# Kernel optimization log

Hardware: AMD Instinct MI355X
Metric: run time of the kernel (lower is better)

## Reference

```python
import jax, jax.numpy as jnp
import numpy as np

NEG_SLOPE = 0.2  # PyG GATConv leaky_relu slope


def _add_self_loops(edge_index, num_nodes):
    loops = jnp.arange(num_nodes, dtype=edge_index.dtype)
    src = jnp.concatenate([edge_index[0], loops])
    dst = jnp.concatenate([edge_index[1], loops])
    return src, dst


def _gat_conv(x, src, dst, W, a_src, a_dst, b, num_nodes):
    # W: [in, H*F]; a_src, a_dst: [H, F]; b: [H*F]
    H, F = a_src.shape
    h = (x @ W).reshape(num_nodes, H, F)                # [N,H,F]
    alpha_src = jnp.einsum('nhf,hf->nh', h, a_src)      # [N,H]
    alpha_dst = jnp.einsum('nhf,hf->nh', h, a_dst)      # [N,H]
    logits = alpha_src[src] + alpha_dst[dst]            # [E,H]
    logits = jax.nn.leaky_relu(logits, NEG_SLOPE)
    # segment softmax over incoming edges of each dst node
    seg_max = jax.ops.segment_max(logits, dst, num_segments=num_nodes)  # [N,H]
    e = jnp.exp(logits - seg_max[dst])                  # [E,H]
    denom = jax.ops.segment_sum(e, dst, num_segments=num_nodes)         # [N,H]
    alpha = e / denom[dst]                              # [E,H] (self-loops guarantee denom>0)
    msg = h[src] * alpha[:, :, None]                    # [E,H,F]
    out = jax.ops.segment_sum(msg, dst, num_segments=num_nodes)         # [N,H,F]
    return out.reshape(num_nodes, H * F) + b            # concat=True


def _gcn_conv(x, src, dst, W, b, num_nodes):
    h = x @ W                                           # [N,out]
    ones = jnp.ones(dst.shape[0], dtype=h.dtype)
    deg = jax.ops.segment_sum(ones, dst, num_segments=num_nodes)        # [N]
    dinv = jnp.where(deg > 0, jax.lax.rsqrt(deg), 0.0)
    norm = dinv[src] * dinv[dst]                        # [E]
    out = jax.ops.segment_sum(h[src] * norm[:, None], dst, num_segments=num_nodes)
    return out + b


def setup_inputs() -> dict:
    key = jax.random.key(0)
    ks = jax.random.split(key, 10)
    N, E = 50000, 800000
    in_dim, hid, H1, ncls = 128, 32, 8, 16
    s = 0.05
    d = {}
    d['x'] = jax.random.normal(ks[0], (N, in_dim), jnp.float32)
    d['edge_index'] = jax.random.randint(ks[1], (2, E), 0, N)
    # GATConv 1: in=128 -> hid=32, heads=8
    d['W1'] = jax.random.normal(ks[2], (in_dim, H1 * hid), jnp.float32) * s
    d['a_src1'] = jax.random.normal(ks[3], (H1, hid), jnp.float32) * s
    d['a_dst1'] = jax.random.normal(ks[4], (H1, hid), jnp.float32) * s
    d['b1'] = jnp.zeros((H1 * hid,), jnp.float32)
    # GATConv 2: in=256 -> hid//2=16, heads=1
    d['W2'] = jax.random.normal(ks[5], (H1 * hid, hid // 2), jnp.float32) * s
    d['a_src2'] = jax.random.normal(ks[6], (1, hid // 2), jnp.float32) * s
    d['a_dst2'] = jax.random.normal(ks[7], (1, hid // 2), jnp.float32) * s
    d['b2'] = jnp.zeros((hid // 2,), jnp.float32)
    # GCNConv: 16 -> 16 classes
    d['W3'] = jax.random.normal(ks[8], (hid // 2, ncls), jnp.float32) * s
    d['b3'] = jnp.zeros((ncls,), jnp.float32)
    return d


def reference(x, edge_index, W1, a_src1, a_dst1, b1, W2, a_src2, a_dst2, b2, W3, b3):
    N = x.shape[0]
    src, dst = _add_self_loops(edge_index, N)
    # dropout layers are identity in eval mode
    h = _gat_conv(x, src, dst, W1, a_src1, a_dst1, b1, N)
    h = jax.nn.elu(h)
    h = _gat_conv(h, src, dst, W2, a_src2, a_dst2, b2, N)
    h = jax.nn.elu(h)
    out = _gcn_conv(h, src, dst, W3, b3, N)
    return out
```

## Files before the change

kernel.cpp:

```cpp
#include <hip/hip_runtime.h>
#include <hip/hip_bf16.h>
#include <math.h>

#define NEG_SLOPE 0.2f
#define DEG_CAP 64

typedef float f32x4 __attribute__((ext_vector_type(4)));
typedef short bf16x8 __attribute__((ext_vector_type(8)));
typedef unsigned int u32x2 __attribute__((ext_vector_type(2)));

static __device__ __forceinline__ float lrelu(float x) { return x > 0.f ? x : NEG_SLOPE * x; }
static __device__ __forceinline__ float elu1(float x)  { return x > 0.f ? x : (expf(x) - 1.f); }

static __device__ __forceinline__ unsigned short f2bf(float x) {
    __hip_bfloat16 h = __float2bfloat16(x);
    return *reinterpret_cast<unsigned short*>(&h);
}
static __device__ __forceinline__ unsigned int pack2bf(float a, float b) {
    return (unsigned int)f2bf(a) | ((unsigned int)f2bf(b) << 16);
}
static __device__ __forceinline__ float bflo(unsigned int u) { return __uint_as_float(u << 16); }
static __device__ __forceinline__ float bfhi(unsigned int u) { return __uint_as_float(u & 0xFFFF0000u); }

__global__ void fill_kernel(const int* __restrict__ ei, int* __restrict__ fillc,
                            int* __restrict__ srcs_p, int E, int E2) {
    int i = blockIdx.x * blockDim.x + threadIdx.x;
    if (i >= E2) return;
    int src, dst;
    if (i < E) { src = ei[i]; dst = ei[E + i]; }
    else       { src = i - E; dst = i - E; }
    int pos = atomicAdd(&fillc[dst], 1);
    if (pos < DEG_CAP) srcs_p[(size_t)dst * DEG_CAP + pos] = src;
}

__global__ __launch_bounds__(256) void prep_kernel(const int* __restrict__ fillc, int* __restrict__ cnts,
                                                   float* __restrict__ dinv, const float* __restrict__ W1,
                                                   unsigned short* __restrict__ Wb, int N) {
    int i = blockIdx.x * 256 + threadIdx.x;
    if (i < N) {
        int c = fillc[i];
        cnts[i] = c < DEG_CAP ? c : DEG_CAP;
        dinv[i] = rsqrtf((float)c);
    }
    if (i < 32768) {
        int j = i & 7, lane = (i >> 3) & 63, t = (i >> 9) & 15, kk = i >> 13;
        int k = kk * 32 + (lane >> 4) * 8 + j;
        int n = t * 16 + (lane & 15);
        Wb[i] = f2bf(W1[k * 256 + n]);
    }
}

__global__ __launch_bounds__(256) void gemm1_kernel(const float* __restrict__ x, const unsigned short* __restrict__ Wb,
                                                    const float* __restrict__ a_src, const float* __restrict__ a_dst,
                                                    unsigned short* __restrict__ h1b, float* __restrict__ as1,
                                                    float* __restrict__ ad1, int M) {
    int w = threadIdx.x >> 6, lane = threadIdx.x & 63;
    int quad = lane >> 4, c = lane & 15;
    int rowA = blockIdx.x * 64 + w * 16 + c;
    int rowAc = rowA < M ? rowA : M - 1;
    f32x4 acc[16];
    #pragma unroll
    for (int t = 0; t < 16; t++) acc[t] = (f32x4){0.f, 0.f, 0.f, 0.f};
    #pragma unroll
    for (int kk = 0; kk < 4; kk++) {
        const float* ap = &x[(size_t)rowAc * 128 + kk * 32 + quad * 8];
        float4 a0 = *(const float4*)ap;
        float4 a1 = *(const float4*)(ap + 4);
        union { bf16x8 v; unsigned int u[4]; } af;
        af.u[0] = pack2bf(a0.x, a0.y); af.u[1] = pack2bf(a0.z, a0.w);
        af.u[2] = pack2bf(a1.x, a1.y); af.u[3] = pack2bf(a1.z, a1.w);
        const bf16x8* bp = (const bf16x8*)&Wb[(size_t)(kk * 16) * 512 + lane * 8];
        #pragma unroll
        for (int t = 0; t < 16; t++) {
            bf16x8 bf = bp[t * 64];
            acc[t] = __builtin_amdgcn_mfma_f32_16x16x32_bf16(af.v, bf, acc[t], 0, 0, 0);
        }
    }
    int growb = blockIdx.x * 64 + w * 16 + quad * 4;
    #pragma unroll
    for (int r = 0; r < 4; r++) {
        int grow = growb + r;
        if (grow < M) {
            #pragma unroll
            for (int t = 0; t < 16; t++)
                h1b[(size_t)grow * 256 + t * 16 + c] = f2bf(acc[t][r]);
        }
    }
    float asA[8], asB[8], adA[8], adB[8];
    #pragma unroll
    for (int h = 0; h < 8; h++) {
        asA[h] = a_src[h * 32 + c];      asB[h] = a_src[h * 32 + 16 + c];
        adA[h] = a_dst[h * 32 + c];      adB[h] = a_dst[h * 32 + 16 + c];
    }
    #pragma unroll
    for (int r = 0; r < 4; r++) {
        int grow = growb + r;
        #pragma unroll
        for (int h = 0; h < 8; h++) {
            float ps = acc[2 * h][r] * asA[h] + acc[2 * h + 1][r] * asB[h];
            float pd = acc[2 * h][r] * adA[h] + acc[2 * h + 1][r] * adB[h];
            ps += __shfl_xor(ps, 1); ps += __shfl_xor(ps, 2); ps += __shfl_xor(ps, 4); ps += __shfl_xor(ps, 8);
            pd += __shfl_xor(pd, 1); pd += __shfl_xor(pd, 2); pd += __shfl_xor(pd, 4); pd += __shfl_xor(pd, 8);
            if (c == 0 && grow < M) { as1[grow * 8 + h] = ps; ad1[grow * 8 + h] = pd; }
        }
    }
}

__global__ __launch_bounds__(256) void agg1_kernel(const unsigned short* __restrict__ h1b, const float* __restrict__ asrc,
                                                   const float* __restrict__ adst, const int* __restrict__ cnts,
                                                   const int* __restrict__ srcs_p, const float* __restrict__ b1,
                                                   unsigned short* __restrict__ h1pb, int N) {
    int node = blockIdx.x * 4 + (threadIdx.x >> 6);
    if (node >= N) return;
    int lane = threadIdx.x & 63;
    int h = lane >> 3, e8 = lane & 7;
    float adn = adst[node * 8 + h];
    int cnt = cnts[node];
    float4 acc = make_float4(0.f, 0.f, 0.f, 0.f);
    float den = 0.f;
    int o4 = lane * 4;
    int sv = srcs_p[node * DEG_CAP + (lane < cnt ? lane : cnt - 1)];
    int g = 0;
    for (; g + 16 <= cnt; g += 16) {
        int ssA = __shfl(sv, g + e8);
        int ssB = __shfl(sv, g + 8 + e8);
        float wA = __expf(lrelu(asrc[ssA * 8 + h] + adn));
        float wB = __expf(lrelu(asrc[ssB * 8 + h] + adn));
        uint2 v[16];
        #pragma unroll
        for (int q = 0; q < 16; q++) {
            int s = __shfl(sv, g + q);
            v[q] = *(const uint2*)&h1b[(size_t)s * 256 + o4];
        }
        #pragma unroll
        for (int q = 0; q < 8; q++) {
            float w = __shfl(wA, (h << 3) | q);
            acc.x += w * bflo(v[q].x); acc.y += w * bfhi(v[q].x);
            acc.z += w * bflo(v[q].y); acc.w += w * bfhi(v[q].y);
            den += w;
        }
        #pragma unroll
        for (int q = 8; q < 16; q++) {
            float w = __shfl(wB, (h << 3) | (q - 8));
            acc.x += w * bflo(v[q].x); acc.y += w * bfhi(v[q].x);
            acc.z += w * bflo(v[q].y); acc.w += w * bfhi(v[q].y);
            den += w;
        }
    }
    if (g + 8 <= cnt) {
        int ss = __shfl(sv, g + e8);
        float wp = __expf(lrelu(asrc[ss * 8 + h] + adn));
        uint2 v[8];
        #pragma unroll
        for (int q = 0; q < 8; q++) {
            int s = __shfl(sv, g + q);
            v[q] = *(const uint2*)&h1b[(size_t)s * 256 + o4];
        }
        #pragma unroll
        for (int q = 0; q < 8; q++) {
            float w = __shfl(wp, (h << 3) | q);
            acc.x += w * bflo(v[q].x); acc.y += w * bfhi(v[q].x);
            acc.z += w * bflo(v[q].y); acc.w += w * bfhi(v[q].y);
            den += w;
        }
        g += 8;
    }
    if (g < cnt) {
        int ep = g + e8;
        int epc = ep < cnt - 1 ? ep : cnt - 1;
        int ss = __shfl(sv, epc);
        float wp = (ep < cnt) ? __expf(lrelu(asrc[ss * 8 + h] + adn)) : 0.f;
        #pragma unroll
        for (int q = 0; q < 8; q++) {
            if (g + q < cnt) {
                int s = __shfl(sv, g + q);
                float w = __shfl(wp, (h << 3) | q);
                uint2 vv = *(const uint2*)&h1b[(size_t)s * 256 + o4];
                acc.x += w * bflo(vv.x); acc.y += w * bfhi(vv.x);
                acc.z += w * bflo(vv.y); acc.w += w * bfhi(vv.y);
                den += w;
            }
        }
    }
    float inv = 1.f / den;
    u32x2 r;
    r.x = pack2bf(elu1(acc.x * inv + b1[o4 + 0]), elu1(acc.y * inv + b1[o4 + 1]));
    r.y = pack2bf(elu1(acc.z * inv + b1[o4 + 2]), elu1(acc.w * inv + b1[o4 + 3]));
    __builtin_nontemporal_store(r, (u32x2*)&h1pb[(size_t)node * 256 + o4]);
}

__global__ __launch_bounds__(256) void gemm2_kernel(const unsigned short* __restrict__ X, const float* __restrict__ W2,
                                                    const float* __restrict__ a_src2, const float* __restrict__ a_dst2,
                                                    float* __restrict__ h2, float* __restrict__ asrc2,
                                                    float* __restrict__ adst2, int N) {
    int lane = threadIdx.x & 63;
    int c = lane & 15, kq = lane >> 4;
    int wid = blockIdx.x * (blockDim.x >> 6) + (threadIdx.x >> 6);
    int nwaves = gridDim.x * (blockDim.x >> 6);
    float w2r[64];
    #pragma unroll
    for (int i = 0; i < 64; i++) w2r[i] = W2[(kq * 64 + i) * 16 + c];
    float as_c = a_src2[c], ad_c = a_dst2[c];
    for (int n = wid; n < N; n += nwaves) {
        const unsigned short* xp = &X[(size_t)n * 256 + kq * 64];
        float acc = 0.f;
        #pragma unroll
        for (int i8 = 0; i8 < 8; i8++) {
            uint4 xv = *(const uint4*)&xp[i8 * 8];
            int b = i8 * 8;
            acc += bflo(xv.x) * w2r[b+0] + bfhi(xv.x) * w2r[b+1]
                 + bflo(xv.y) * w2r[b+2] + bfhi(xv.y) * w2r[b+3]
                 + bflo(xv.z) * w2r[b+4] + bfhi(xv.z) * w2r[b+5]
                 + bflo(xv.w) * w2r[b+6] + bfhi(xv.w) * w2r[b+7];
        }
        acc += __shfl_xor(acc, 16);
        acc += __shfl_xor(acc, 32);
        float s1 = acc * as_c, s2 = acc * ad_c;
        #pragma unroll
        for (int off = 1; off < 16; off <<= 1) { s1 += __shfl_xor(s1, off); s2 += __shfl_xor(s2, off); }
        if (kq == 0) h2[n * 16 + c] = acc;
        if (lane == 0) { asrc2[n] = s1; adst2[n] = s2; }
    }
}

__global__ __launch_bounds__(256) void agg2_kernel(const float* __restrict__ h2, const float* __restrict__ asrc2,
                                                   const float* __restrict__ adst2, const int* __restrict__ cnts,
                                                   const int* __restrict__ srcs_p, const float* __restrict__ b2,
                                                   const float* __restrict__ W3, float* __restrict__ h4, int N) {
    int node = blockIdx.x * 4 + (threadIdx.x >> 6);
    if (node >= N) return;
    int lane = threadIdx.x & 63;
    int q = lane >> 4, c = lane & 15;
    float adn = adst2[node];
    int cnt = cnts[node];
    float acc = 0.f, den = 0.f;
    int sv = 0; float wv = 0.f;
    if (lane < cnt) { sv = srcs_p[node * DEG_CAP + lane]; wv = __expf(lrelu(asrc2[sv] + adn)); }
    int nit = (cnt + 3) >> 2;
    int it = 0;
    for (; it + 4 <= nit; it += 4) {
        int s0 = __shfl(sv, it * 4 + q),       s1 = __shfl(sv, (it + 1) * 4 + q);
        int s2 = __shfl(sv, (it + 2) * 4 + q), s3 = __shfl(sv, (it + 3) * 4 + q);
        float w0 = __shfl(wv, it * 4 + q),       w1 = __shfl(wv, (it + 1) * 4 + q);
        float w2 = __shfl(wv, (it + 2) * 4 + q), w3 = __shfl(wv, (it + 3) * 4 + q);
        float v0 = h2[s0 * 16 + c], v1 = h2[s1 * 16 + c];
        float v2 = h2[s2 * 16 + c], v3 = h2[s3 * 16 + c];
        acc += w0 * v0 + w1 * v1 + w2 * v2 + w3 * v3;
        den += (w0 + w1) + (w2 + w3);
    }
    for (; it < nit; it++) {
        int j = it * 4 + q;
        int s = __shfl(sv, j);
        float w = __shfl(wv, j);
        acc += w * h2[s * 16 + c]; den += w;
    }
    acc += __shfl_xor(acc, 16); acc += __shfl_xor(acc, 32);
    den += __shfl_xor(den, 16); den += __shfl_xor(den, 32);
    float h3v = elu1(acc / den + b2[c]);
    float h4v = 0.f;
    #pragma unroll
    for (int cs = 0; cs < 16; cs++) {
        float hv = __shfl(h3v, cs);
        h4v += hv * W3[cs * 16 + c];
    }
    if (q == 0) h4[node * 16 + c] = h4v;
}

__global__ __launch_bounds__(256) void agg3_kernel(const float* __restrict__ h4, const float* __restrict__ dinv,
                                                   const int* __restrict__ cnts, const int* __restrict__ srcs_p,
                                                   const float* __restrict__ b3, float* __restrict__ out, int N) {
    int node = blockIdx.x * 4 + (threadIdx.x >> 6);
    if (node >= N) return;
    int lane = threadIdx.x & 63;
    int q = lane >> 4, c = lane & 15;
    int cnt = cnts[node];
    float acc = 0.f;
    int sv = 0; float wv = 0.f;
    if (lane < cnt) { sv = srcs_p[node * DEG_CAP + lane]; wv = dinv[sv]; }
    int nit = (cnt + 3) >> 2;
    int it = 0;
    for (; it + 4 <= nit; it += 4) {
        int s0 = __shfl(sv, it * 4 + q),       s1 = __shfl(sv, (it + 1) * 4 + q);
        int s2 = __shfl(sv, (it + 2) * 4 + q), s3 = __shfl(sv, (it + 3) * 4 + q);
        float w0 = __shfl(wv, it * 4 + q),       w1 = __shfl(wv, (it + 1) * 4 + q);
        float w2 = __shfl(wv, (it + 2) * 4 + q), w3 = __shfl(wv, (it + 3) * 4 + q);
        float v0 = h4[s0 * 16 + c], v1 = h4[s1 * 16 + c];
        float v2 = h4[s2 * 16 + c], v3 = h4[s3 * 16 + c];
        acc += w0 * v0 + w1 * v1 + w2 * v2 + w3 * v3;
    }
    for (; it < nit; it++) {
        int j = it * 4 + q;
        int s = __shfl(sv, j);
        float w = __shfl(wv, j);
        acc += w * h4[s * 16 + c];
    }
    acc += __shfl_xor(acc, 16); acc += __shfl_xor(acc, 32);
    if (q == 0) out[node * 16 + c] = acc * dinv[node] + b3[c];
}

extern "C" void kernel_launch(void* const* d_in, const int* in_sizes, int n_in,
                              void* d_out, int out_size, void* d_ws, size_t ws_size,
                              hipStream_t stream) {
    const float* x      = (const float*)d_in[0];
    const int*   ei     = (const int*)d_in[1];
    const float* W1     = (const float*)d_in[2];
    const float* a_src1 = (const float*)d_in[3];
    const float* a_dst1 = (const float*)d_in[4];
    const float* b1     = (const float*)d_in[5];
    const float* W2     = (const float*)d_in[6];
    const float* a_src2 = (const float*)d_in[7];
    const float* a_dst2 = (const float*)d_in[8];
    const float* b2     = (const float*)d_in[9];
    const float* W3     = (const float*)d_in[10];
    const float* b3     = (const float*)d_in[11];
    float* out = (float*)d_out;

    const int N  = in_sizes[0] / 128;
    const int E  = in_sizes[1] / 2;
    const int E2 = E + N;

    char* p = (char*)d_ws;
    auto alloc = [&](size_t bytes) -> void* {
        void* r = (void*)p;
        p += (bytes + 255) & ~(size_t)255;
        return r;
    };
    int*   fillc  = (int*)alloc((size_t)N * 4);
    int*   cnts   = (int*)alloc((size_t)N * 4);
    int*   srcs_p = (int*)alloc((size_t)N * DEG_CAP * 4);
    unsigned short* Wb   = (unsigned short*)alloc((size_t)32768 * 2);
    unsigned short* h1b  = (unsigned short*)alloc((size_t)N * 256 * 2);
    unsigned short* h1pb = (unsigned short*)alloc((size_t)N * 256 * 2);
    float* as1    = (float*)alloc((size_t)N * 8 * 4);
    float* ad1    = (float*)alloc((size_t)N * 8 * 4);
    float* h2     = (float*)alloc((size_t)N * 16 * 4);
    float* as2    = (float*)alloc((size_t)N * 4);
    float* ad2    = (float*)alloc((size_t)N * 4);
    float* h4     = (float*)alloc((size_t)N * 16 * 4);
    float* dinv   = (float*)alloc((size_t)N * 4);

    (void)hipMemsetAsync(fillc, 0, (size_t)N * 4, stream);
    fill_kernel<<<(E2 + 255) / 256, 256, 0, stream>>>(ei, fillc, srcs_p, E, E2);
    prep_kernel<<<(N + 255) / 256, 256, 0, stream>>>(fillc, cnts, dinv, W1, Wb, N);

    gemm1_kernel<<<(N + 63) / 64, 256, 0, stream>>>(x, Wb, a_src1, a_dst1, h1b, as1, ad1, N);
    agg1_kernel<<<(N + 3) / 4, 256, 0, stream>>>(h1b, as1, ad1, cnts, srcs_p, b1, h1pb, N);

    gemm2_kernel<<<1024, 256, 0, stream>>>(h1pb, W2, a_src2, a_dst2, h2, as2, ad2, N);
    agg2_kernel<<<(N + 3) / 4, 256, 0, stream>>>(h2, as2, ad2, cnts, srcs_p, b2, W3, h4, N);

    agg3_kernel<<<(N + 3) / 4, 256, 0, stream>>>(h4, dinv, cnts, srcs_p, b3, out, N);
}
```

Before: 314.0 us.

## Pad degree counters, drop prep kernel, vectorize agg2/agg3 gathers with float4

Degree counters are padded to one per 64-byte stride so the edge-fill atomics stop contending on shared cache lines. The memset and prep kernel are replaced by an init kernel plus on-the-fly degree clamping, and dinv moves into gemm2. agg2 and agg3 now gather 16-float rows with float4 loads, 16 edges per pass, then reduce across lanes with xor shuffles. The padding makes the counter array 16x larger, which adds memory traffic when it is read in later kernels.

Result: slower. 325.4 us (+3.6%).

```diff
diff --git a/kernel.cpp b/kernel.cpp
--- a/kernel.cpp
+++ b/kernel.cpp
@@ -4,6 +4,7 @@
 
 #define NEG_SLOPE 0.2f
 #define DEG_CAP 64
+#define FPAD 16
 
 typedef float f32x4 __attribute__((ext_vector_type(4)));
 typedef short bf16x8 __attribute__((ext_vector_type(8)));
@@ -22,32 +23,27 @@
 static __device__ __forceinline__ float bflo(unsigned int u) { return __uint_as_float(u << 16); }
 static __device__ __forceinline__ float bfhi(unsigned int u) { return __uint_as_float(u & 0xFFFF0000u); }
 
-__global__ void fill_kernel(const int* __restrict__ ei, int* __restrict__ fillc,
+__global__ __launch_bounds__(256) void init_kernel(int* __restrict__ fillc_p, const float* __restrict__ W1,
+                                                   unsigned short* __restrict__ Wb, int N) {
+    int i = blockIdx.x * 256 + threadIdx.x;
+    if (i < N) fillc_p[i * FPAD] = 0;
+    if (i < 32768) {
+        int j = i & 7, lane = (i >> 3) & 63, t = (i >> 9) & 15, kk = i >> 13;
+        int k = kk * 32 + (lane >> 4) * 8 + j;
+        int n = t * 16 + (lane & 15);
+        Wb[i] = f2bf(W1[k * 256 + n]);
+    }
+}
+
+__global__ void fill_kernel(const int* __restrict__ ei, int* __restrict__ fillc_p,
                             int* __restrict__ srcs_p, int E, int E2) {
     int i = blockIdx.x * blockDim.x + threadIdx.x;
     if (i >= E2) return;
     int src, dst;
     if (i < E) { src = ei[i]; dst = ei[E + i]; }
     else       { src = i - E; dst = i - E; }
-    int pos = atomicAdd(&fillc[dst], 1);
+    int pos = atomicAdd(&fillc_p[(size_t)dst * FPAD], 1);
     if (pos < DEG_CAP) srcs_p[(size_t)dst * DEG_CAP + pos] = src;
-}
-
-__global__ __launch_bounds__(256) void prep_kernel(const int* __restrict__ fillc, int* __restrict__ cnts,
-                                                   float* __restrict__ dinv, const float* __restrict__ W1,
-                                                   unsigned short* __restrict__ Wb, int N) {
-    int i = blockIdx.x * 256 + threadIdx.x;
-    if (i < N) {
-        int c = fillc[i];
-        cnts[i] = c < DEG_CAP ? c : DEG_CAP;
-        dinv[i] = rsqrtf((float)c);
-    }
-    if (i < 32768) {
-        int j = i & 7, lane = (i >> 3) & 63, t = (i >> 9) & 15, kk = i >> 13;
-        int k = kk * 32 + (lane >> 4) * 8 + j;
-        int n = t * 16 + (lane & 15);
-        Wb[i] = f2bf(W1[k * 256 + n]);
-    }
 }
 
 __global__ __launch_bounds__(256) void gemm1_kernel(const float* __restrict__ x, const unsigned short* __restrict__ Wb,
@@ -107,7 +103,7 @@
 }
 
 __global__ __launch_bounds__(256) void agg1_kernel(const unsigned short* __restrict__ h1b, const float* __restrict__ asrc,
-                                                   const float* __restrict__ adst, const int* __restrict__ cnts,
+                                                   const float* __restrict__ adst, const int* __restrict__ fillc_p,
                                                    const int* __restrict__ srcs_p, const float* __restrict__ b1,
                                                    unsigned short* __restrict__ h1pb, int N) {
     int node = blockIdx.x * 4 + (threadIdx.x >> 6);
@@ -115,7 +111,8 @@
     int lane = threadIdx.x & 63;
     int h = lane >> 3, e8 = lane & 7;
     float adn = adst[node * 8 + h];
-    int cnt = cnts[node];
+    int deg = fillc_p[(size_t)node * FPAD];
+    int cnt = deg < DEG_CAP ? deg : DEG_CAP;
     float4 acc = make_float4(0.f, 0.f, 0.f, 0.f);
     float den = 0.f;
     int o4 = lane * 4;
@@ -191,8 +188,9 @@
 
 __global__ __launch_bounds__(256) void gemm2_kernel(const unsigned short* __restrict__ X, const float* __restrict__ W2,
                                                     const float* __restrict__ a_src2, const float* __restrict__ a_dst2,
-                                                    float* __restrict__ h2, float* __restrict__ asrc2,
-                                                    float* __restrict__ adst2, int N) {
+                                                    const int* __restrict__ fillc_p, float* __restrict__ h2,
+                                                    float* __restrict__ asrc2, float* __restrict__ adst2,
+                                                    float* __restrict__ dinv, int N) {
     int lane = threadIdx.x & 63;
     int c = lane & 15, kq = lane >> 4;
     int wid = blockIdx.x * (blockDim.x >> 6) + (threadIdx.x >> 6);
@@ -219,83 +217,97 @@
         #pragma unroll
         for (int off = 1; off < 16; off <<= 1) { s1 += __shfl_xor(s1, off); s2 += __shfl_xor(s2, off); }
         if (kq == 0) h2[n * 16 + c] = acc;
-        if (lane == 0) { asrc2[n] = s1; adst2[n] = s2; }
+        if (lane == 0) {
+            asrc2[n] = s1; adst2[n] = s2;
+            dinv[n] = rsqrtf((float)fillc_p[(size_t)n * FPAD]);
+        }
     }
 }
 
 __global__ __launch_bounds__(256) void agg2_kernel(const float* __restrict__ h2, const float* __restrict__ asrc2,
-                                                   const float* __restrict__ adst2, const int* __restrict__ cnts,
+                                                   const float* __restrict__ adst2, const int* __restrict__ fillc_p,
                                                    const int* __restrict__ srcs_p, const float* __restrict__ b2,
                                                    const float* __restrict__ W3, float* __restrict__ h4, int N) {
     int node = blockIdx.x * 4 + (threadIdx.x >> 6);
     if (node >= N) return;
     int lane = threadIdx.x & 63;
-    int q = lane >> 4, c = lane & 15;
+    int e16 = lane >> 2, seg = lane & 3;
     float adn = adst2[node];
-    int cnt = cnts[node];
-    float acc = 0.f, den = 0.f;
-    int sv = 0; float wv = 0.f;
-    if (lane < cnt) { sv = srcs_p[node * DEG_CAP + lane]; wv = __expf(lrelu(asrc2[sv] + adn)); }
-    int nit = (cnt + 3) >> 2;
-    int it = 0;
-    for (; it + 4 <= nit; it += 4) {
-        int s0 = __shfl(sv, it * 4 + q),       s1 = __shfl(sv, (it + 1) * 4 + q);
-        int s2 = __shfl(sv, (it + 2) * 4 + q), s3 = __shfl(sv, (it + 3) * 4 + q);
-        float w0 = __shfl(wv, it * 4 + q),       w1 = __shfl(wv, (it + 1) * 4 + q);
-        float w2 = __shfl(wv, (it + 2) * 4 + q), w3 = __shfl(wv, (it + 3) * 4 + q);
-        float v0 = h2[s0 * 16 + c], v1 = h2[s1 * 16 + c];
-        float v2 = h2[s2 * 16 + c], v3 = h2[s3 * 16 + c];
-        acc += w0 * v0 + w1 * v1 + w2 * v2 + w3 * v3;
-        den += (w0 + w1) + (w2 + w3);
-    }
-    for (; it < nit; it++) {
-        int j = it * 4 + q;
-        int s = __shfl(sv, j);
-        float w = __shfl(wv, j);
-        acc += w * h2[s * 16 + c]; den += w;
-    }
-    acc += __shfl_xor(acc, 16); acc += __shfl_xor(acc, 32);
-    den += __shfl_xor(den, 16); den += __shfl_xor(den, 32);
-    float h3v = elu1(acc / den + b2[c]);
+    int deg = fillc_p[(size_t)node * FPAD];
+    int cnt = deg < DEG_CAP ? deg : DEG_CAP;
+    int sv = srcs_p[node * DEG_CAP + (lane < cnt ? lane : cnt - 1)];
+    float wv = (lane < cnt) ? __expf(lrelu(asrc2[sv] + adn)) : 0.f;
+    float4 acc = make_float4(0.f, 0.f, 0.f, 0.f);
+    float den = 0.f;
+    #pragma unroll
+    for (int r = 0; r < 4; r++) {
+        if (r * 16 < cnt) {
+            int j = r * 16 + e16;
+            int s = __shfl(sv, j);
+            float w = __shfl(wv, j);
+            const float4 v = *(const float4*)&h2[(size_t)s * 16 + seg * 4];
+            acc.x += w * v.x; acc.y += w * v.y; acc.z += w * v.z; acc.w += w * v.w;
+            den += w;
+        }
+    }
+    #pragma unroll
+    for (int off = 4; off < 64; off <<= 1) {
+        acc.x += __shfl_xor(acc.x, off); acc.y += __shfl_xor(acc.y, off);
+        acc.z += __shfl_xor(acc.z, off); acc.w += __shfl_xor(acc.w, off);
+        den += __shfl_xor(den, off);
+    }
+    float inv = 1.f / den;
+    float h3v[4];
+    h3v[0] = elu1(acc.x * inv + b2[seg * 4 + 0]);
+    h3v[1] = elu1(acc.y * inv + b2[seg * 4 + 1]);
+    h3v[2] = elu1(acc.z * inv + b2[seg * 4 + 2]);
+    h3v[3] = elu1(acc.w * inv + b2[seg * 4 + 3]);
+    int c = lane & 15;
     float h4v = 0.f;
     #pragma unroll
     for (int cs = 0; cs < 16; cs++) {
-        float hv = __shfl(h3v, cs);
+        float hv = __shfl(h3v[cs & 3], cs >> 2);
         h4v += hv * W3[cs * 16 + c];
     }
-    if (q == 0) h4[node * 16 + c] = h4v;
+    if (lane < 16) h4[node * 16 + c] = h4v;
 }
 
 __global__ __launch_bounds__(256) void agg3_kernel(const float* __restrict__ h4, const float* __restrict__ dinv,
-                                                   const int* __restrict__ cnts, const int* __restrict__ srcs_p,
+                                                   const int* __restrict__ fillc_p, const int* __restrict__ srcs_p,
                                                    const float* __restrict__ b3, float* __restrict__ out, int N) {
     int node = blockIdx.x * 4 + (threadIdx.x >> 6);
     if (node >= N) return;
     int lane = threadIdx.x & 63;
-    int q = lane >> 4, c = lane & 15;
-    int cnt = cnts[node];
-    float acc = 0.f;
-    int sv = 0; float wv = 0.f;
-    if (lane < cnt) { sv = srcs_p[node * DEG_CAP + lane]; wv = dinv[sv]; }
-    int nit = (cnt + 3) >> 2;
-    int it = 0;
-    for (; it + 4 <= nit; it += 4) {
-        int s0 = __shfl(sv, it * 4 + q),       s1 = __shfl(sv, (it + 1) * 4 + q);
-        int s2 = __shfl(sv, (it + 2) * 4 + q), s3 = __shfl(sv, (it + 3) * 4 + q);
-        float w0 = __shfl(wv, it * 4 + q),       w1 = __shfl(wv, (it + 1) * 4 + q);
-        float w2 = __shfl(wv, (it + 2) * 4 + q), w3 = __shfl(wv, (it + 3) * 4 + q);
-        float v0 = h4[s0 * 16 + c], v1 = h4[s1 * 16 + c];
-        float v2 = h4[s2 * 16 + c], v3 = h4[s3 * 16 + c];
-        acc += w0 * v0 + w1 * v1 + w2 * v2 + w3 * v3;
-    }
-    for (; it < nit; it++) {
-        int j = it * 4 + q;
-        int s = __shfl(sv, j);
-        float w = __shfl(wv, j);
-        acc += w * h4[s * 16 + c];
-    }
-    acc += __shfl_xor(acc, 16); acc += __shfl_xor(acc, 32);
-    if (q == 0) out[node * 16 + c] = acc * dinv[node] + b3[c];
+    int e16 = lane >> 2, seg = lane & 3;
+    int deg = fillc_p[(size_t)node * FPAD];
+    int cnt = deg < DEG_CAP ? deg : DEG_CAP;
+    int sv = srcs_p[node * DEG_CAP + (lane < cnt ? lane : cnt - 1)];
+    float wv = (lane < cnt) ? dinv[sv] : 0.f;
+    float4 acc = make_float4(0.f, 0.f, 0.f, 0.f);
+    #pragma unroll
+    for (int r = 0; r < 4; r++) {
+        if (r * 16 < cnt) {
+            int j = r * 16 + e16;
+            int s = __shfl(sv, j);
+            float w = __shfl(wv, j);
+            const float4 v = *(const float4*)&h4[(size_t)s * 16 + seg * 4];
+            acc.x += w * v.x; acc.y += w * v.y; acc.z += w * v.z; acc.w += w * v.w;
+        }
+    }
+    #pragma unroll
+    for (int off = 4; off < 64; off <<= 1) {
+        acc.x += __shfl_xor(acc.x, off); acc.y += __shfl_xor(acc.y, off);
+        acc.z += __shfl_xor(acc.z, off); acc.w += __shfl_xor(acc.w, off);
+    }
+    if (lane < 4) {
+        float dn = dinv[node];
+        float4 r;
+        r.x = acc.x * dn + b3[seg * 4 + 0];
+        r.y = acc.y * dn + b3[seg * 4 + 1];
+        r.z = acc.z * dn + b3[seg * 4 + 2];
+        r.w = acc.w * dn + b3[seg * 4 + 3];
+        *(float4*)&out[(size_t)node * 16 + seg * 4] = r;
+    }
 }
 
 extern "C" void kernel_launch(void* const* d_in, const int* in_sizes, int n_in,
@@ -325,9 +337,8 @@
         p += (bytes + 255) & ~(size_t)255;
         return r;
     };
-    int*   fillc  = (int*)alloc((size_t)N * 4);
-    int*   cnts   = (int*)alloc((size_t)N * 4);
-    int*   srcs_p = (int*)alloc((size_t)N * DEG_CAP * 4);
+    int*   fillc_p = (int*)alloc((size_t)N * FPAD * 4);
+    int*   srcs_p  = (int*)alloc((size_t)N * DEG_CAP * 4);
     unsigned short* Wb   = (unsigned short*)alloc((size_t)32768 * 2);
     unsigned short* h1b  = (unsigned short*)alloc((size_t)N * 256 * 2);
     unsigned short* h1pb = (unsigned short*)alloc((size_t)N * 256 * 2);
@@ -339,15 +350,14 @@
     float* h4     = (float*)alloc((size_t)N * 16 * 4);
     float* dinv   = (float*)alloc((size_t)N * 4);
 
-    (void)hipMemsetAsync(fillc, 0, (size_t)N * 4, stream);
-    fill_kernel<<<(E2 + 255) / 256, 256, 0, stream>>>(ei, fillc, srcs_p, E, E2);
-    prep_kernel<<<(N + 255) / 256, 256, 0, stream>>>(fillc, cnts, dinv, W1, Wb, N);
+    init_kernel<<<(N + 255) / 256, 256, 0, stream>>>(fillc_p, W1, Wb, N);
+    fill_kernel<<<(E2 + 255) / 256, 256, 0, stream>>>(ei, fillc_p, srcs_p, E, E2);
 
     gemm1_kernel<<<(N + 63) / 64, 256, 0, stream>>>(x, Wb, a_src1, a_dst1, h1b, as1, ad1, N);
-    agg1_kernel<<<(N + 3) / 4, 256, 0, stream>>>(h1b, as1, ad1, cnts, srcs_p, b1, h1pb, N);
-
-    gemm2_kernel<<<1024, 256, 0, stream>>>(h1pb, W2, a_src2, a_dst2, h2, as2, ad2, N);
-    agg2_kernel<<<(N + 3) / 4, 256, 0, stream>>>(h2, as2, ad2, cnts, srcs_p, b2, W3, h4, N);
-
-    agg3_kernel<<<(N + 3) / 4, 256, 0, stream>>>(h4, dinv, cnts, srcs_p, b3, out, N);
-}
+    agg1_kernel<<<(N + 3) / 4, 256, 0, stream>>>(h1b, as1, ad1, fillc_p, srcs_p, b1, h1pb, N);
+
+    gemm2_kernel<<<1024, 256, 0, stream>>>(h1pb, W2, a_src2, a_dst2, fillc_p, h2, as2, ad2, dinv, N);
+    agg2_kernel<<<(N + 3) / 4, 256, 0, stream>>>(h2, as2, ad2, fillc_p, srcs_p, b2, W3, h4, N);
+
+    agg3_kernel<<<(N + 3) / 4, 256, 0, stream>>>(h4, dinv, fillc_p, srcs_p, b3, out, N);
+}
```
